# Optimization experiments

Measured on AMD Instinct MI355X. Metric: run time of the kernel, lower is better.

Reference implementation:

```python
import jax, jax.numpy as jnp
import numpy as np

N_NODES = 4096
IN_FEAT = 256
N_HEADS = 8
N_HIDDEN = 32  # out_features // n_heads
NEG_SLOPE = 0.2


def setup_inputs() -> dict:
    key = jax.random.key(0)
    k1, k2, k3, k4 = jax.random.split(key, 4)
    h = jax.random.normal(k1, (N_NODES, IN_FEAT), dtype=jnp.float32)
    W = jax.random.normal(k2, (N_HEADS * N_HIDDEN, IN_FEAT), dtype=jnp.float32) * 0.05
    a = jax.random.normal(k3, (2 * N_HIDDEN,), dtype=jnp.float32) * 0.05
    adj_mat = jax.random.randint(k4, (N_NODES, N_NODES, 1), 0, 2, dtype=jnp.int32)
    return {"h": h, "W": W, "a": a, "adj_mat": adj_mat}


def reference(h, W, a, adj_mat):
    n = h.shape[0]
    # g = linear(h) -> [N, H, F]
    g = (h @ W.T).reshape(n, N_HEADS, N_HIDDEN)
    # e_ij = LeakyReLU(a^T [g_i || g_j]) = LeakyReLU(a_l . g_i + a_r . g_j)
    a_l, a_r = a[:N_HIDDEN], a[N_HIDDEN:]
    s_i = jnp.einsum('nhf,f->nh', g, a_l)  # destination term (repeat_interleave axis)
    s_j = jnp.einsum('nhf,f->nh', g, a_r)  # source term (repeat axis)
    e = jax.nn.leaky_relu(s_i[:, None, :] + s_j[None, :, :], NEG_SLOPE)  # [N, N, H]
    e = jnp.where(adj_mat == 0, jnp.float32(-jnp.inf), e)
    att = jax.nn.softmax(e, axis=1)  # softmax over source nodes j
    # dropout(p) in eval mode -> identity
    out = jnp.einsum('ijh,jhf->ihf', att, g)
    return out.reshape(n, N_HEADS * N_HIDDEN)  # is_concat=True
```

## Files before the change

### kernel.cpp

```cpp
#include <hip/hip_runtime.h>
#include <hip/hip_bf16.h>
#include <math.h>

constexpr int N   = 4096;
constexpr int F   = 256;
constexpr int NH  = 8;
constexpr int HID = 32;
constexpr float SLOPE = 0.2f;

using frag_ab = __attribute__((ext_vector_type(8))) short;
using frag_cd = __attribute__((ext_vector_type(4))) float;

__device__ inline unsigned short f2bf(float x) {
  unsigned int u = __float_as_uint(x);
  unsigned int r = (u + 0x7fffu + ((u >> 16) & 1u)) >> 16;
  return (unsigned short)r;
}

__global__ __launch_bounds__(256) void k_pre(const float* __restrict__ h,
                                             const float* __restrict__ W,
                                             const float* __restrict__ a,
                                             const int* __restrict__ adj,
                                             unsigned short* __restrict__ hb,
                                             float* __restrict__ U,
                                             unsigned int* __restrict__ bits,
                                             float* __restrict__ outp,
                                             float* __restrict__ lbuf) {
  const int b = blockIdx.x, t = threadIdx.x;
  if (b < 544) {
    const int idx8 = (b * 256 + t) * 8;
    const float* src = (idx8 < N * F) ? (h + idx8) : (W + idx8 - N * F);
    const float4 v0 = *(const float4*)src;
    const float4 v1 = *(const float4*)(src + 4);
    unsigned short tmp[8];
    tmp[0] = f2bf(v0.x); tmp[1] = f2bf(v0.y); tmp[2] = f2bf(v0.z); tmp[3] = f2bf(v0.w);
    tmp[4] = f2bf(v1.x); tmp[5] = f2bf(v1.y); tmp[6] = f2bf(v1.z); tmp[7] = f2bf(v1.w);
    *(int4*)(hb + idx8) = *(int4*)tmp;
  } else if (b < 560) {
    const int c = b - 544, k = t;
    const int head = c & 7, side = c >> 3;
    float acc = 0.f;
#pragma unroll
    for (int f = 0; f < 32; ++f)
      acc += W[(size_t)(head * 32 + f) * F + k] * a[side * 32 + f];
    U[c * F + k] = acc;
  } else if (b < 1584) {
    const int lane = t & 63, wv = t >> 6;
    const int row = (b - 560) * 4 + wv;
    const int4* arow = (const int4*)(adj + (size_t)row * N);
#pragma unroll
    for (int c = 0; c < 16; ++c) {
      const int4 av = arow[c * 64 + lane];
      unsigned int v = (av.x != 0 ? 1u : 0u) | (av.y != 0 ? 2u : 0u) |
                       (av.z != 0 ? 4u : 0u) | (av.w != 0 ? 8u : 0u);
      v <<= ((lane & 7) * 4);
      v |= __shfl_xor(v, 1);
      v |= __shfl_xor(v, 2);
      v |= __shfl_xor(v, 4);
      if ((lane & 7) == 0) bits[(size_t)row * (N / 32) + c * 8 + (lane >> 3)] = v;
    }
  } else if (b < 2608) {
    *(float4*)(outp + ((size_t)(b - 1584) * 256 + t) * 4) =
        make_float4(0.f, 0.f, 0.f, 0.f);
  } else {
    *(float4*)(lbuf + ((size_t)(b - 2608) * 256 + t) * 4) =
        make_float4(0.f, 0.f, 0.f, 0.f);
  }
}

__global__ __launch_bounds__(256) void k_mid(const float* __restrict__ h,
                                             const float* __restrict__ U,
                                             const unsigned short* __restrict__ hb,
                                             const unsigned short* __restrict__ Wb,
                                             float* __restrict__ RT,
                                             float* __restrict__ BT,
                                             float* __restrict__ DT,
                                             unsigned short* __restrict__ gT) {
  __shared__ float hs[16][260];
  __shared__ float Us[16][260];
  const int b = blockIdx.x, t = threadIdx.x;
  if (b < 256) {
    const int i0 = b * 16;
    {
      const int r = t >> 4, s0 = (t & 15) * 16;
      const float4* src = (const float4*)(h + (size_t)(i0 + r) * F + s0);
      const float4* usr = (const float4*)(U + (size_t)r * F + s0);
#pragma unroll
      for (int q = 0; q < 4; ++q) {
        *(float4*)&hs[r][s0 + q * 4] = src[q];
        *(float4*)&Us[r][s0 + q * 4] = usr[q];
      }
    }
    __syncthreads();
    const int r = t >> 4, c = t & 15;
    float acc = 0.f;
#pragma unroll
    for (int k4 = 0; k4 < 64; ++k4) {
      const float4 hv = *(const float4*)&hs[r][k4 * 4];
      const float4 uv = *(const float4*)&Us[c][k4 * 4];
      acc += hv.x * uv.x + hv.y * uv.y + hv.z * uv.z + hv.w * uv.w;
    }
    const int n = i0 + r;
    if (c < 8) {
      RT[(size_t)n * NH + c] = __expf(-0.8f * acc);
    } else {
      const int hd = c - 8;
      BT[(size_t)hd * N + n] = __expf(acc);
      DT[(size_t)hd * N + n] = __expf(SLOPE * acc);
    }
  } else {
    const int lane = t & 63;
    const int tile = (b - 256) * 4 + (t >> 6);
    const int mt = tile >> 4, nt = tile & 15;
    const int m0 = mt * 16, n0 = nt * 16;
    const int n16 = lane & 15, quad = lane >> 4;
    frag_cd acc = {0.f, 0.f, 0.f, 0.f};
    const unsigned short* ap = hb + (size_t)(m0 + n16) * F + quad * 8;
    const unsigned short* bp = Wb + (size_t)(n0 + n16) * F + quad * 8;
#pragma unroll
    for (int ks = 0; ks < F / 32; ++ks) {
      const frag_ab af = *(const frag_ab*)(ap + ks * 32);
      const frag_ab bf = *(const frag_ab*)(bp + ks * 32);
      acc = __builtin_amdgcn_mfma_f32_16x16x32_bf16(af, bf, acc, 0, 0, 0);
    }
    unsigned short tmp[4];
#pragma unroll
    for (int reg = 0; reg < 4; ++reg) tmp[reg] = f2bf(acc[reg]);
    *(int2*)(gT + (size_t)(n0 + n16) * N + m0 + quad * 4) = *(int2*)tmp;
  }
}

constexpr int TI = 32;
constexpr int NSPLIT = 4;

__global__ __launch_bounds__(256, 6) void k_agg(
    const unsigned short* __restrict__ gT,
    const float* __restrict__ RT,
    const float* __restrict__ BT, const float* __restrict__ DT,
    const unsigned int* __restrict__ bits,
    float* __restrict__ outp, float* __restrict__ lbuf) {
  __shared__ __align__(16) unsigned short sB[64][140];

  const int t    = threadIdx.x;
  const int lane = t & 63;
  const int wv   = t >> 6;
  const int isub = wv & 1;
  const int hh   = wv >> 1;
  const int b    = blockIdx.x;
  const int hp   = b & 3;
  const int js   = (b >> 2) & (NSPLIT - 1);
  const int i0   = (b >> 4) * TI;
  const int head = hp * 2 + hh;

  const int n16  = lane & 15;
  const int quad = lane >> 4;

  const int myi  = i0 + isub * 16 + n16;
  const float Ri = RT[(size_t)myi * NH + head];

  const float* Bp = BT + (size_t)head * N + js * 1024;
  const float* Dp = DT + (size_t)head * N + js * 1024;
  const uint4* bp4 = (const uint4*)(bits + (size_t)myi * (N / 32) + js * 32);

  frag_cd acc0 = {0.f, 0.f, 0.f, 0.f};
  frag_cd acc1 = {0.f, 0.f, 0.f, 0.f};
  frag_cd accl = {0.f, 0.f, 0.f, 0.f};
  frag_ab fone;
#pragma unroll
  for (int u = 0; u < 8; ++u) fone[u] = (short)0x3F80;

  const int sr = t >> 2, ss0 = t & 3;

  for (int c8 = 0; c8 < 8; ++c8) {
    const int j0 = c8 * 128;
    __syncthreads();
    {
      const unsigned short* src = gT + (size_t)(hp * 64 + sr) * N + js * 1024 + j0;
#pragma unroll
      for (int s = 0; s < 4; ++s) {
        const int seg = ss0 + s * 4;
        *(int4*)&sB[sr][seg * 8] = *(const int4*)(src + seg * 8);
      }
    }
    const uint4 bw = bp4[c8];
    __syncthreads();
#pragma unroll
    for (int ks = 0; ks < 4; ++ks) {
      const int lo  = ks * 32 + quad * 8;
      const int off = j0 + lo;
      const float4 B0 = *(const float4*)(Bp + off);
      const float4 B1 = *(const float4*)(Bp + off + 4);
      const float4 D0 = *(const float4*)(Dp + off);
      const float4 D1 = *(const float4*)(Dp + off + 4);
      const frag_ab b0 = *(const frag_ab*)&sB[hh * 32 + n16][lo];
      const frag_ab b1 = *(const frag_ab*)&sB[hh * 32 + 16 + n16][lo];
      const unsigned int word = ks == 0 ? bw.x : ks == 1 ? bw.y : ks == 2 ? bw.z : bw.w;
      const unsigned int mb = (word >> (quad * 8)) & 0xffu;

      const float Bu[8] = {B0.x, B0.y, B0.z, B0.w, B1.x, B1.y, B1.z, B1.w};
      const float Du[8] = {D0.x, D0.y, D0.z, D0.w, D1.x, D1.y, D1.z, D1.w};
      int packed[4];
#pragma unroll
      for (int p = 0; p < 4; ++p) {
        float w0 = fmaxf(Bu[2 * p],     Ri * Du[2 * p]);
        float w1 = fmaxf(Bu[2 * p + 1], Ri * Du[2 * p + 1]);
        w0 = (mb & (1u << (2 * p)))     ? w0 : 0.f;
        w1 = (mb & (1u << (2 * p + 1))) ? w1 : 0.f;
        const __hip_bfloat162 bp2 = __float22bfloat162_rn(make_float2(w0, w1));
        __builtin_memcpy(&packed[p], &bp2, 4);
      }
      frag_ab af;
      __builtin_memcpy(&af, packed, 16);
      acc0 = __builtin_amdgcn_mfma_f32_16x16x32_bf16(af, b0, acc0, 0, 0, 0);
      acc1 = __builtin_amdgcn_mfma_f32_16x16x32_bf16(af, b1, acc1, 0, 0, 0);
      accl = __builtin_amdgcn_mfma_f32_16x16x32_bf16(af, fone, accl, 0, 0, 0);
    }
  }
#pragma unroll
  for (int reg = 0; reg < 4; ++reg) {
    const int row = quad * 4 + reg;
    const int gi = i0 + isub * 16 + row;
    atomicAdd(&outp[(size_t)gi * F + head * HID + n16], acc0[reg]);
    atomicAdd(&outp[(size_t)gi * F + head * HID + 16 + n16], acc1[reg]);
    if (n16 == 0) atomicAdd(&lbuf[(size_t)gi * NH + head], accl[reg]);
  }
}

__global__ __launch_bounds__(256) void k_norm(float* __restrict__ outp,
                                              const float* __restrict__ lbuf) {
  const int idx = blockIdx.x * 256 + threadIdx.x;
  const int i = idx >> 6, fq = idx & 63;
  const int hh = fq >> 3;
  const float inv = 1.f / lbuf[(size_t)i * NH + hh];
  float4 v = *(float4*)(outp + (size_t)idx * 4);
  v.x *= inv; v.y *= inv; v.z *= inv; v.w *= inv;
  *(float4*)(outp + (size_t)idx * 4) = v;
}

extern "C" void kernel_launch(void* const* d_in, const int* in_sizes, int n_in,
                              void* d_out, int out_size, void* d_ws, size_t ws_size,
                              hipStream_t stream) {
  const float* h   = (const float*)d_in[0];
  const float* W   = (const float*)d_in[1];
  const float* a   = (const float*)d_in[2];
  const int*   adj = (const int*)d_in[3];
  float* out = (float*)d_out;

  char* ws = (char*)d_ws;
  unsigned short* hb = (unsigned short*)ws;  ws += (size_t)(N * F + F * F) * 2;
  unsigned short* Wb = hb + (size_t)N * F;
  unsigned short* gT = (unsigned short*)ws;  ws += (size_t)N * F * 2;
  unsigned int* bits = (unsigned int*)ws;    ws += (size_t)N * (N / 32) * 4;
  float* U    = (float*)ws;                  ws += 16 * F * 4;
  float* RT   = (float*)ws;                  ws += (size_t)N * NH * 4;
  float* BT   = (float*)ws;                  ws += (size_t)N * NH * 4;
  float* DT   = (float*)ws;                  ws += (size_t)N * NH * 4;
  float* lbuf = (float*)ws;                  ws += (size_t)N * NH * 4;

  k_pre<<<dim3(2640), dim3(256), 0, stream>>>(h, W, a, adj, hb, U, bits, out, lbuf);
  k_mid<<<dim3(1280), dim3(256), 0, stream>>>(h, U, hb, Wb, RT, BT, DT, gT);
  k_agg<<<dim3((N / TI) * 4 * NSPLIT), dim3(256), 0, stream>>>(
      gT, RT, BT, DT, bits, out, lbuf);
  k_norm<<<dim3(N * F / 4 / 256), dim3(256), 0, stream>>>(out, lbuf);
}
```

Baseline: 184.8 us.

## Use 32x32 MFMA in aggregation with packed bf16 B/D staged in LDS

The aggregation kernel switches from three 16x16x32 MFMAs per step to a single 32x32x16 MFMA per wave. Waves now split the j range and merge their partial results through shared memory before the atomics. The softmax denominator is summed in scalar registers rather than by a ones-vector MFMA. The exp factors B and D are packed as bf16 pairs into one word and staged through LDS, and the adjacency bit-packing and zeroing work in k_pre is redistributed across more blocks. This cuts MFMA count, global loads and atomics, at the cost of lower precision for B and D and an extra LDS merge with barriers.

After: 164.0 us. -11.3%, faster.

```diff
diff --git a/kernel.cpp b/kernel.cpp
--- a/kernel.cpp
+++ b/kernel.cpp
@@ -8,8 +8,9 @@
 constexpr int HID = 32;
 constexpr float SLOPE = 0.2f;
 
-using frag_ab = __attribute__((ext_vector_type(8))) short;
-using frag_cd = __attribute__((ext_vector_type(4))) float;
+using frag_ab  = __attribute__((ext_vector_type(8))) short;
+using frag_cd  = __attribute__((ext_vector_type(4))) float;
+using frag_c16 = __attribute__((ext_vector_type(16))) float;
 
 __device__ inline unsigned short f2bf(float x) {
   unsigned int u = __float_as_uint(x);
@@ -44,12 +45,14 @@
     for (int f = 0; f < 32; ++f)
       acc += W[(size_t)(head * 32 + f) * F + k] * a[side * 32 + f];
     U[c * F + k] = acc;
-  } else if (b < 1584) {
-    const int lane = t & 63, wv = t >> 6;
-    const int row = (b - 560) * 4 + wv;
-    const int4* arow = (const int4*)(adj + (size_t)row * N);
-#pragma unroll
-    for (int c = 0; c < 16; ++c) {
+  } else if (b < 2608) {
+    const int lane = t & 63, w = t >> 6;
+    const int row  = (b - 560) * 2 + (w >> 1);
+    const int half = w & 1;
+    const int4* arow = (const int4*)(adj + (size_t)row * N) + half * 512;
+    unsigned int* brow = bits + (size_t)row * (N / 32) + half * 64;
+#pragma unroll
+    for (int c = 0; c < 8; ++c) {
       const int4 av = arow[c * 64 + lane];
       unsigned int v = (av.x != 0 ? 1u : 0u) | (av.y != 0 ? 2u : 0u) |
                        (av.z != 0 ? 4u : 0u) | (av.w != 0 ? 8u : 0u);
@@ -57,13 +60,16 @@
       v |= __shfl_xor(v, 1);
       v |= __shfl_xor(v, 2);
       v |= __shfl_xor(v, 4);
-      if ((lane & 7) == 0) bits[(size_t)row * (N / 32) + c * 8 + (lane >> 3)] = v;
-    }
-  } else if (b < 2608) {
-    *(float4*)(outp + ((size_t)(b - 1584) * 256 + t) * 4) =
-        make_float4(0.f, 0.f, 0.f, 0.f);
+      if ((lane & 7) == 0) brow[c * 8 + (lane >> 3)] = v;
+    }
+  } else if (b < 2864) {
+    const int base = (b - 2608) * 256 + t;
+#pragma unroll
+    for (int q = 0; q < 4; ++q)
+      *(float4*)(outp + ((size_t)q * 65536 + base) * 4) =
+          make_float4(0.f, 0.f, 0.f, 0.f);
   } else {
-    *(float4*)(lbuf + ((size_t)(b - 2608) * 256 + t) * 4) =
+    *(float4*)(lbuf + ((size_t)(b - 2864) * 256 + t) * 4) =
         make_float4(0.f, 0.f, 0.f, 0.f);
   }
 }
@@ -73,8 +79,7 @@
                                              const unsigned short* __restrict__ hb,
                                              const unsigned short* __restrict__ Wb,
                                              float* __restrict__ RT,
-                                             float* __restrict__ BT,
-                                             float* __restrict__ DT,
+                                             unsigned int* __restrict__ BDT,
                                              unsigned short* __restrict__ gT) {
   __shared__ float hs[16][260];
   __shared__ float Us[16][260];
@@ -105,8 +110,9 @@
       RT[(size_t)n * NH + c] = __expf(-0.8f * acc);
     } else {
       const int hd = c - 8;
-      BT[(size_t)hd * N + n] = __expf(acc);
-      DT[(size_t)hd * N + n] = __expf(SLOPE * acc);
+      const unsigned int bw = f2bf(__expf(acc));
+      const unsigned int dw = f2bf(__expf(SLOPE * acc));
+      BDT[(size_t)hd * N + n] = (bw << 16) | dw;
     }
   } else {
     const int lane = t & 63;
@@ -136,93 +142,116 @@
 __global__ __launch_bounds__(256, 6) void k_agg(
     const unsigned short* __restrict__ gT,
     const float* __restrict__ RT,
-    const float* __restrict__ BT, const float* __restrict__ DT,
+    const unsigned int* __restrict__ BDT,
     const unsigned int* __restrict__ bits,
     float* __restrict__ outp, float* __restrict__ lbuf) {
   __shared__ __align__(16) unsigned short sB[64][140];
+  __shared__ __align__(16) unsigned int sBD[2][128];
 
   const int t    = threadIdx.x;
   const int lane = t & 63;
   const int wv   = t >> 6;
-  const int isub = wv & 1;
-  const int hh   = wv >> 1;
+  const int hd   = wv >> 1;
+  const int jh   = wv & 1;
   const int b    = blockIdx.x;
   const int hp   = b & 3;
   const int js   = (b >> 2) & (NSPLIT - 1);
   const int i0   = (b >> 4) * TI;
-  const int head = hp * 2 + hh;
-
-  const int n16  = lane & 15;
-  const int quad = lane >> 4;
-
-  const int myi  = i0 + isub * 16 + n16;
+  const int head = hp * 2 + hd;
+
+  const int n32 = lane & 31;
+  const int kh  = lane >> 5;
+
+  const int myi  = i0 + n32;
   const float Ri = RT[(size_t)myi * NH + head];
-
-  const float* Bp = BT + (size_t)head * N + js * 1024;
-  const float* Dp = DT + (size_t)head * N + js * 1024;
   const uint4* bp4 = (const uint4*)(bits + (size_t)myi * (N / 32) + js * 32);
 
-  frag_cd acc0 = {0.f, 0.f, 0.f, 0.f};
-  frag_cd acc1 = {0.f, 0.f, 0.f, 0.f};
-  frag_cd accl = {0.f, 0.f, 0.f, 0.f};
-  frag_ab fone;
-#pragma unroll
-  for (int u = 0; u < 8; ++u) fone[u] = (short)0x3F80;
+  frag_c16 acc = {0.f, 0.f, 0.f, 0.f, 0.f, 0.f, 0.f, 0.f,
+                  0.f, 0.f, 0.f, 0.f, 0.f, 0.f, 0.f, 0.f};
+  float lpart = 0.f;
 
   const int sr = t >> 2, ss0 = t & 3;
+  const unsigned short* gsrc = gT + (size_t)(hp * 64 + sr) * N + js * 1024;
+  const unsigned int*  bdsrc = BDT + (size_t)(hp * 2 + (t >> 7)) * N + js * 1024 + (t & 127);
 
   for (int c8 = 0; c8 < 8; ++c8) {
-    const int j0 = c8 * 128;
     __syncthreads();
     {
-      const unsigned short* src = gT + (size_t)(hp * 64 + sr) * N + js * 1024 + j0;
 #pragma unroll
       for (int s = 0; s < 4; ++s) {
         const int seg = ss0 + s * 4;
-        *(int4*)&sB[sr][seg * 8] = *(const int4*)(src + seg * 8);
+        const int4 v = *(const int4*)(gsrc + c8 * 128 + seg * 8);
+        *(int2*)&sB[sr][seg * 8]     = make_int2(v.x, v.y);
+        *(int2*)&sB[sr][seg * 8 + 4] = make_int2(v.z, v.w);
       }
     }
+    sBD[t >> 7][t & 127] = bdsrc[c8 * 128];
     const uint4 bw = bp4[c8];
     __syncthreads();
 #pragma unroll
-    for (int ks = 0; ks < 4; ++ks) {
-      const int lo  = ks * 32 + quad * 8;
-      const int off = j0 + lo;
-      const float4 B0 = *(const float4*)(Bp + off);
-      const float4 B1 = *(const float4*)(Bp + off + 4);
-      const float4 D0 = *(const float4*)(Dp + off);
-      const float4 D1 = *(const float4*)(Dp + off + 4);
-      const frag_ab b0 = *(const frag_ab*)&sB[hh * 32 + n16][lo];
-      const frag_ab b1 = *(const frag_ab*)&sB[hh * 32 + 16 + n16][lo];
-      const unsigned int word = ks == 0 ? bw.x : ks == 1 ? bw.y : ks == 2 ? bw.z : bw.w;
-      const unsigned int mb = (word >> (quad * 8)) & 0xffu;
-
-      const float Bu[8] = {B0.x, B0.y, B0.z, B0.w, B1.x, B1.y, B1.z, B1.w};
-      const float Du[8] = {D0.x, D0.y, D0.z, D0.w, D1.x, D1.y, D1.z, D1.w};
+    for (int sh = 0; sh < 4; ++sh) {
+      const int ss = sh * 2 + jh;
+      const int jb = ss * 16 + kh * 8;
+      const uint4 bdl = *(const uint4*)&sBD[hd][jb];
+      const uint4 bdh = *(const uint4*)&sBD[hd][jb + 4];
+      const unsigned int w32 =
+          (ss >> 1) == 0 ? bw.x : (ss >> 1) == 1 ? bw.y : (ss >> 1) == 2 ? bw.z : bw.w;
+      const unsigned int mb = (w32 >> (((ss & 1) << 4) + (kh << 3))) & 0xFFu;
+
+      const unsigned int bdw[8] = {bdl.x, bdl.y, bdl.z, bdl.w,
+                                   bdh.x, bdh.y, bdh.z, bdh.w};
       int packed[4];
 #pragma unroll
       for (int p = 0; p < 4; ++p) {
-        float w0 = fmaxf(Bu[2 * p],     Ri * Du[2 * p]);
-        float w1 = fmaxf(Bu[2 * p + 1], Ri * Du[2 * p + 1]);
+        const unsigned int u0 = bdw[2 * p], u1 = bdw[2 * p + 1];
+        const float B0 = __uint_as_float(u0 & 0xFFFF0000u);
+        const float D0 = __uint_as_float(u0 << 16);
+        const float B1 = __uint_as_float(u1 & 0xFFFF0000u);
+        const float D1 = __uint_as_float(u1 << 16);
+        float w0 = fmaxf(B0, Ri * D0);
+        float w1 = fmaxf(B1, Ri * D1);
         w0 = (mb & (1u << (2 * p)))     ? w0 : 0.f;
         w1 = (mb & (1u << (2 * p + 1))) ? w1 : 0.f;
+        lpart += w0 + w1;
         const __hip_bfloat162 bp2 = __float22bfloat162_rn(make_float2(w0, w1));
         __builtin_memcpy(&packed[p], &bp2, 4);
       }
       frag_ab af;
       __builtin_memcpy(&af, packed, 16);
-      acc0 = __builtin_amdgcn_mfma_f32_16x16x32_bf16(af, b0, acc0, 0, 0, 0);
-      acc1 = __builtin_amdgcn_mfma_f32_16x16x32_bf16(af, b1, acc1, 0, 0, 0);
-      accl = __builtin_amdgcn_mfma_f32_16x16x32_bf16(af, fone, accl, 0, 0, 0);
-    }
-  }
-#pragma unroll
-  for (int reg = 0; reg < 4; ++reg) {
-    const int row = quad * 4 + reg;
-    const int gi = i0 + isub * 16 + row;
-    atomicAdd(&outp[(size_t)gi * F + head * HID + n16], acc0[reg]);
-    atomicAdd(&outp[(size_t)gi * F + head * HID + 16 + n16], acc1[reg]);
-    if (n16 == 0) atomicAdd(&lbuf[(size_t)gi * NH + head], accl[reg]);
+
+      const int frow = hd * 32 + n32;
+      const int2 blo = *(const int2*)&sB[frow][jb];
+      const int2 bhi = *(const int2*)&sB[frow][jb + 4];
+      const int bt[4] = {blo.x, blo.y, bhi.x, bhi.y};
+      frag_ab bf;
+      __builtin_memcpy(&bf, bt, 16);
+
+      acc = __builtin_amdgcn_mfma_f32_32x32x16_bf16(af, bf, acc, 0, 0, 0);
+    }
+  }
+
+  float* mrg  = (float*)&sB[0][0];
+  float* mrgl = (float*)&sBD[0][0];
+  const float lp2 = lpart + __shfl_xor(lpart, 32);
+  __syncthreads();
+  if (jh == 1) {
+#pragma unroll
+    for (int reg = 0; reg < 16; ++reg) {
+      const int row = (reg & 3) + 8 * (reg >> 2) + 4 * kh;
+      mrg[(size_t)(hd * 32 + row) * 32 + n32] = acc[reg];
+    }
+    if (kh == 0) mrgl[hd * 32 + n32] = lp2;
+  }
+  __syncthreads();
+  if (jh == 0) {
+    const float lt = lp2 + mrgl[hd * 32 + n32];
+    if (kh == 0) atomicAdd(&lbuf[(size_t)(i0 + n32) * NH + head], lt);
+#pragma unroll
+    for (int reg = 0; reg < 16; ++reg) {
+      const int row = (reg & 3) + 8 * (reg >> 2) + 4 * kh;
+      const float v = acc[reg] + mrg[(size_t)(hd * 32 + row) * 32 + n32];
+      atomicAdd(&outp[(size_t)(i0 + row) * F + head * HID + n32], v);
+    }
   }
 }
 
@@ -253,13 +282,12 @@
   unsigned int* bits = (unsigned int*)ws;    ws += (size_t)N * (N / 32) * 4;
   float* U    = (float*)ws;                  ws += 16 * F * 4;
   float* RT   = (float*)ws;                  ws += (size_t)N * NH * 4;
-  float* BT   = (float*)ws;                  ws += (size_t)N * NH * 4;
-  float* DT   = (float*)ws;                  ws += (size_t)N * NH * 4;
+  unsigned int* BDT = (unsigned int*)ws;     ws += (size_t)N * NH * 4;
   float* lbuf = (float*)ws;                  ws += (size_t)N * NH * 4;
 
-  k_pre<<<dim3(2640), dim3(256), 0, stream>>>(h, W, a, adj, hb, U, bits, out, lbuf);
-  k_mid<<<dim3(1280), dim3(256), 0, stream>>>(h, U, hb, Wb, RT, BT, DT, gT);
+  k_pre<<<dim3(2896), dim3(256), 0, stream>>>(h, W, a, adj, hb, U, bits, out, lbuf);
+  k_mid<<<dim3(1280), dim3(256), 0, stream>>>(h, U, hb, Wb, RT, BDT, gT);
   k_agg<<<dim3((N / TI) * 4 * NSPLIT), dim3(256), 0, stream>>>(
-      gT, RT, BT, DT, bits, out, lbuf);
+      gT, RT, BDT, bits, out, lbuf);
   k_norm<<<dim3(N * F / 4 / 256), dim3(256), 0, stream>>>(out, lbuf);
 }
```
